# Performance work log

Hardware: AMD Instinct MI355X
Metric: run time of the kernel (lower is better)

## Reference

```python
import jax, jax.numpy as jnp
import numpy as np

B, D, C = 2048, 1024, 8192


def setup_inputs() -> dict:
    key = jax.random.key(0)
    k1, k2, k3 = jax.random.split(key, 3)
    x = jax.random.normal(k1, (B, D), dtype=jnp.float32)
    y = jax.random.randint(k2, (B,), 0, C)
    centroids = jax.random.normal(k3, (C, D), dtype=jnp.float32)
    return {"x": x, "y": y, "centroids": centroids}


def reference(x, y, centroids):
    x2 = jnp.sum(x * x, axis=-1, keepdims=True)          # (B, 1)
    c2 = jnp.sum(centroids * centroids, axis=-1)          # (C,)
    logits = -(x2 + c2[None, :] - 2.0 * (x @ centroids.T))  # (B, C)
    decisions = jnp.argmax(logits, axis=1)                # nearest centroid
    score = jnp.mean((decisions == y).astype(jnp.float32))
    # CrossEntropyLoss(distances, y)
    logp = jax.nn.log_softmax(logits, axis=-1)
    loss = -jnp.mean(jnp.take_along_axis(logp, y[:, None], axis=1))
    return loss, score
```

## Files before the change

kernel.cpp:

```cpp
#include <hip/hip_runtime.h>
#include <cstdint>

#define MDIM 2048
#define KDIM 1024
#define CDIM 8192
#define BM 128
#define BN 128
#define BK 32
#define NCHUNK (2 * (CDIM / BN))

typedef __attribute__((ext_vector_type(8))) __bf16 bf16x8;
typedef __attribute__((ext_vector_type(4))) float f32x4;

__device__ __forceinline__ unsigned short f2bf(float f) {
  unsigned u = __float_as_uint(f);
  u += 0x7fffu + ((u >> 16) & 1u);
  return (unsigned short)(u >> 16);
}

__device__ __forceinline__ void async_ld16(const void* g, void* l) {
  __builtin_amdgcn_global_load_lds(
      (__attribute__((address_space(1))) void*)(g),
      (__attribute__((address_space(3))) void*)(l),
      16, 0, 0);
}

__global__ __launch_bounds__(256) void convert_all(const float* __restrict__ x,
                                                   const float* __restrict__ cent,
                                                   unsigned short* __restrict__ xb,
                                                   unsigned short* __restrict__ cb,
                                                   float* __restrict__ c2) {
  const int b = blockIdx.x, t = threadIdx.x;
  if (b < MDIM) {
    const float4 v = ((const float4*)(x + (size_t)b * KDIM))[t];
    ushort4 o;
    o.x = f2bf(v.x); o.y = f2bf(v.y); o.z = f2bf(v.z); o.w = f2bf(v.w);
    ((ushort4*)(xb + (size_t)b * KDIM))[t] = o;
  } else {
    const int row = b - MDIM;
    const float4 v = ((const float4*)(cent + (size_t)row * KDIM))[t];
    ushort4 o;
    o.x = f2bf(v.x); o.y = f2bf(v.y); o.z = f2bf(v.z); o.w = f2bf(v.w);
    ((ushort4*)(cb + (size_t)row * KDIM))[t] = o;
    float p = v.x * v.x + v.y * v.y + v.z * v.z + v.w * v.w;
    for (int d = 32; d; d >>= 1) p += __shfl_down(p, d, 64);
    __shared__ float red[4];
    if ((t & 63) == 0) red[t >> 6] = p;
    __syncthreads();
    if (t == 0) c2[row] = red[0] + red[1] + red[2] + red[3];
  }
}

__global__ __launch_bounds__(256) void gemm_reduce(
    const unsigned short* __restrict__ Ab, const unsigned short* __restrict__ Bb,
    const float* __restrict__ c2,
    float* __restrict__ pm, float* __restrict__ pl, int* __restrict__ pidx) {
  __shared__ __align__(16) unsigned short As[BM * BK];
  __shared__ __align__(16) unsigned short Bs[BN * BK];
  const int tid = threadIdx.x;
  const int wave = tid >> 6, lane = tid & 63;
  const int wm = wave >> 1, wn = wave & 1;
  const int bn = blockIdx.x, bm = blockIdx.y;
  const int quad = lane >> 4, c16 = lane & 15;

  f32x4 acc[4][4] = {};

  const int srow = lane >> 2;
  const int scol = (lane & 3) * 8;
  const unsigned short* ag = Ab + (size_t)(bm * BM + wave * 32 + srow) * KDIM + scol;
  const unsigned short* bg = Bb + (size_t)(bn * BN + wave * 32 + srow) * KDIM + scol;
  unsigned short* asl = &As[(wave * 32) * BK];
  unsigned short* bsl = &Bs[(wave * 32) * BK];

  for (int k0 = 0; k0 < KDIM; k0 += BK) {
    async_ld16(ag + k0, asl);
    async_ld16(ag + k0 + 16 * KDIM, asl + 16 * BK);
    async_ld16(bg + k0, bsl);
    async_ld16(bg + k0 + 16 * KDIM, bsl + 16 * BK);
    __syncthreads();
    bf16x8 a[4], b[4];
#pragma unroll
    for (int mt = 0; mt < 4; ++mt)
      a[mt] = *(const bf16x8*)&As[(wm * 64 + mt * 16 + c16) * BK + quad * 8];
#pragma unroll
    for (int nt = 0; nt < 4; ++nt)
      b[nt] = *(const bf16x8*)&Bs[(wn * 64 + nt * 16 + c16) * BK + quad * 8];
#pragma unroll
    for (int mt = 0; mt < 4; ++mt)
#pragma unroll
      for (int nt = 0; nt < 4; ++nt)
        acc[mt][nt] = __builtin_amdgcn_mfma_f32_16x16x32_bf16(a[mt], b[nt], acc[mt][nt], 0, 0, 0);
    __syncthreads();
  }

  const int colbase = bn * BN + wn * 64;
  float c2v[4];
#pragma unroll
  for (int nt = 0; nt < 4; ++nt) c2v[nt] = c2[colbase + nt * 16 + c16];

  const int chunk = bn * 2 + wn;
#pragma unroll
  for (int mt = 0; mt < 4; ++mt) {
#pragma unroll
    for (int r = 0; r < 4; ++r) {
      float sv[4];
#pragma unroll
      for (int nt = 0; nt < 4; ++nt) sv[nt] = 2.0f * acc[mt][nt][r] - c2v[nt];
      float m = sv[0];
      int idx = colbase + c16;
#pragma unroll
      for (int nt = 1; nt < 4; ++nt) {
        if (sv[nt] > m) { m = sv[nt]; idx = colbase + nt * 16 + c16; }
      }
      float l = 0.f;
#pragma unroll
      for (int nt = 0; nt < 4; ++nt) l += __expf(sv[nt] - m);
      for (int d = 1; d < 16; d <<= 1) {
        float om = __shfl_xor(m, d, 64);
        float ol = __shfl_xor(l, d, 64);
        int oi = __shfl_xor(idx, d, 64);
        float M = fmaxf(m, om);
        l = l * __expf(m - M) + ol * __expf(om - M);
        idx = (om > m || (om == m && oi < idx)) ? oi : idx;
        m = M;
      }
      if (c16 == 0) {
        const int row = bm * BM + wm * 64 + mt * 16 + quad * 4 + r;
        pm[(size_t)row * NCHUNK + chunk] = m;
        pl[(size_t)row * NCHUNK + chunk] = l;
        pidx[(size_t)row * NCHUNK + chunk] = idx;
      }
    }
  }
}

__global__ __launch_bounds__(128) void combine_kernel(
    const float* __restrict__ pm, const float* __restrict__ pl,
    const int* __restrict__ pidx, const float* __restrict__ x,
    const float* __restrict__ cent, const float* __restrict__ c2,
    const int* __restrict__ y,
    float* __restrict__ loss_part, float* __restrict__ corr_part) {
  const int row = blockIdx.x, t = threadIdx.x;
  const int yc = y[row];

  float m = pm[(size_t)row * NCHUNK + t];
  float l = pl[(size_t)row * NCHUNK + t];
  int idx = pidx[(size_t)row * NCHUNK + t];

  const float4* xa = (const float4*)(x + (size_t)row * KDIM) + t * 2;
  const float4* ca = (const float4*)(cent + (size_t)yc * KDIM) + t * 2;
  const float4 a0 = xa[0], a1 = xa[1], b0 = ca[0], b1 = ca[1];
  float dot = a0.x * b0.x + a0.y * b0.y + a0.z * b0.z + a0.w * b0.w
            + a1.x * b1.x + a1.y * b1.y + a1.z * b1.z + a1.w * b1.w;

  for (int d = 1; d < 64; d <<= 1) {
    const float om = __shfl_xor(m, d, 64);
    const float ol = __shfl_xor(l, d, 64);
    const int oi = __shfl_xor(idx, d, 64);
    const float od = __shfl_xor(dot, d, 64);
    const float M = fmaxf(m, om);
    l = l * __expf(m - M) + ol * __expf(om - M);
    idx = (om > m || (om == m && oi < idx)) ? oi : idx;
    m = M;
    dot += od;
  }
  __shared__ float sm[2], sl[2], sd[2];
  __shared__ int si[2];
  if ((t & 63) == 0) { sm[t >> 6] = m; sl[t >> 6] = l; si[t >> 6] = idx; sd[t >> 6] = dot; }
  __syncthreads();
  if (t == 0) {
    const float m0 = sm[0], m1 = sm[1];
    const float M = fmaxf(m0, m1);
    const float L = sl[0] * __expf(m0 - M) + sl[1] * __expf(m1 - M);
    int g;
    if (m1 > m0 || (m1 == m0 && si[1] < si[0])) g = si[1]; else g = si[0];
    const float sy = 2.0f * (sd[0] + sd[1]) - c2[yc];
    loss_part[row] = __logf(L) + M - sy;
    corr_part[row] = (g == yc) ? 1.f : 0.f;
  }
}

__global__ __launch_bounds__(256) void finalize(const float* __restrict__ loss_part,
                                                const float* __restrict__ corr_part,
                                                float* __restrict__ out) {
  const int t = threadIdx.x;
  float s0 = 0.f, s1 = 0.f;
  for (int i = t; i < MDIM; i += 256) { s0 += loss_part[i]; s1 += corr_part[i]; }
  for (int d = 32; d; d >>= 1) {
    s0 += __shfl_down(s0, d, 64);
    s1 += __shfl_down(s1, d, 64);
  }
  __shared__ float r0[4], r1[4];
  if ((t & 63) == 0) { r0[t >> 6] = s0; r1[t >> 6] = s1; }
  __syncthreads();
  if (t == 0) {
    out[0] = (r0[0] + r0[1] + r0[2] + r0[3]) * (1.0f / MDIM);
    out[1] = (r1[0] + r1[1] + r1[2] + r1[3]) * (1.0f / MDIM);
  }
}

extern "C" void kernel_launch(void* const* d_in, const int* in_sizes, int n_in,
                              void* d_out, int out_size, void* d_ws, size_t ws_size,
                              hipStream_t stream) {
  const float* x = (const float*)d_in[0];
  const int* y = (const int*)d_in[1];
  const float* cent = (const float*)d_in[2];
  float* out = (float*)d_out;

  char* ws = (char*)d_ws;
  const size_t OFF_XB = 0;
  const size_t OFF_CB = OFF_XB + (size_t)MDIM * KDIM * 2;
  const size_t OFF_C2 = OFF_CB + (size_t)CDIM * KDIM * 2;
  const size_t OFF_PM = OFF_C2 + (size_t)CDIM * 4;
  const size_t OFF_PL = OFF_PM + (size_t)NCHUNK * MDIM * 4;
  const size_t OFF_PI = OFF_PL + (size_t)NCHUNK * MDIM * 4;
  const size_t OFF_LP = OFF_PI + (size_t)NCHUNK * MDIM * 4;
  const size_t OFF_CP = OFF_LP + (size_t)MDIM * 4;
  const size_t NEED = OFF_CP + (size_t)MDIM * 4;
  if (ws_size < NEED) return;

  unsigned short* xb = (unsigned short*)(ws + OFF_XB);
  unsigned short* cb = (unsigned short*)(ws + OFF_CB);
  float* c2 = (float*)(ws + OFF_C2);
  float* pm = (float*)(ws + OFF_PM);
  float* pl = (float*)(ws + OFF_PL);
  int* pidx = (int*)(ws + OFF_PI);
  float* loss_part = (float*)(ws + OFF_LP);
  float* corr_part = (float*)(ws + OFF_CP);

  convert_all<<<MDIM + CDIM, 256, 0, stream>>>(x, cent, xb, cb, c2);
  gemm_reduce<<<dim3(CDIM / BN, MDIM / BM), 256, 0, stream>>>(xb, cb, c2, pm, pl, pidx);
  combine_kernel<<<MDIM, 128, 0, stream>>>(pm, pl, pidx, x, cent, c2, y, loss_part, corr_part);
  finalize<<<1, 256, 0, stream>>>(loss_part, corr_part, out);
}
```

Baseline: 153.6 us.

## Use 256x256 tiles with 4-stage async LDS pipeline, swizzle, and block remap

The GEMM moves to 256x256 block tiles with 512 threads. A 4-deep ring of LDS buffers is filled by asynchronous global-to-LDS loads three steps ahead, with explicit vmcnt waits and a single barrier per k-step, so memory latency overlaps MFMA work. LDS rows use an XOR swizzle to avoid bank conflicts, and the block index is remapped so that neighbouring blocks share tiles in L2. NCHUNK stays at 128, so combine is unchanged. The costs are 128KB of LDS, larger register use and fewer blocks in the grid (256 blocks).

```diff
diff --git a/kernel.cpp b/kernel.cpp
--- a/kernel.cpp
+++ b/kernel.cpp
@@ -4,10 +4,11 @@
 #define MDIM 2048
 #define KDIM 1024
 #define CDIM 8192
-#define BM 128
-#define BN 128
+#define BM 256
+#define BN 256
 #define BK 32
-#define NCHUNK (2 * (CDIM / BN))
+#define NT (KDIM / BK)
+#define NCHUNK (CDIM / 64)
 
 typedef __attribute__((ext_vector_type(8))) __bf16 bf16x8;
 typedef __attribute__((ext_vector_type(4))) float f32x4;
@@ -51,56 +52,93 @@
   }
 }
 
-__global__ __launch_bounds__(256) void gemm_reduce(
+__global__ __launch_bounds__(512, 2) void gemm_reduce(
     const unsigned short* __restrict__ Ab, const unsigned short* __restrict__ Bb,
     const float* __restrict__ c2,
     float* __restrict__ pm, float* __restrict__ pl, int* __restrict__ pidx) {
-  __shared__ __align__(16) unsigned short As[BM * BK];
-  __shared__ __align__(16) unsigned short Bs[BN * BK];
+  __shared__ __align__(16) char lds[4 * 32768];
+
   const int tid = threadIdx.x;
   const int wave = tid >> 6, lane = tid & 63;
-  const int wm = wave >> 1, wn = wave & 1;
-  const int bn = blockIdx.x, bm = blockIdx.y;
+  const int wm = wave >> 2, wn = wave & 3;
   const int quad = lane >> 4, c16 = lane & 15;
 
-  f32x4 acc[4][4] = {};
-
-  const int srow = lane >> 2;
-  const int scol = (lane & 3) * 8;
-  const unsigned short* ag = Ab + (size_t)(bm * BM + wave * 32 + srow) * KDIM + scol;
-  const unsigned short* bg = Bb + (size_t)(bn * BN + wave * 32 + srow) * KDIM + scol;
-  unsigned short* asl = &As[(wave * 32) * BK];
-  unsigned short* bsl = &Bs[(wave * 32) * BK];
-
-  for (int k0 = 0; k0 < KDIM; k0 += BK) {
-    async_ld16(ag + k0, asl);
-    async_ld16(ag + k0 + 16 * KDIM, asl + 16 * BK);
-    async_ld16(bg + k0, bsl);
-    async_ld16(bg + k0 + 16 * KDIM, bsl + 16 * BK);
-    __syncthreads();
-    bf16x8 a[4], b[4];
-#pragma unroll
-    for (int mt = 0; mt < 4; ++mt)
-      a[mt] = *(const bf16x8*)&As[(wm * 64 + mt * 16 + c16) * BK + quad * 8];
-#pragma unroll
-    for (int nt = 0; nt < 4; ++nt)
-      b[nt] = *(const bf16x8*)&Bs[(wn * 64 + nt * 16 + c16) * BK + quad * 8];
-#pragma unroll
-    for (int mt = 0; mt < 4; ++mt)
+  const int id = blockIdx.y * gridDim.x + blockIdx.x;
+  const int lid = (id & 7) * 32 + (id >> 3);
+  const int bm = lid >> 5, bn = lid & 31;
+  const int bmBase = bm * BM, bnBase = bn * BN;
+
+  const int r1 = tid >> 2, c1 = (tid & 3) ^ ((r1 >> 1) & 3);
+  const int r2 = (tid + 512) >> 2, c2s = (tid & 3) ^ ((r2 >> 1) & 3);
+  const char* Ag1 = (const char*)(Ab + (size_t)(bmBase + r1) * KDIM + c1 * 8);
+  const char* Ag2 = (const char*)(Ab + (size_t)(bmBase + r2) * KDIM + c2s * 8);
+  const char* Bg1 = (const char*)(Bb + (size_t)(bnBase + r1) * KDIM + c1 * 8);
+  const char* Bg2 = (const char*)(Bb + (size_t)(bnBase + r2) * KDIM + c2s * 8);
+  const int wbyte = wave * 1024;
+
+  int aoff[8], boff[4];
+#pragma unroll
+  for (int mt = 0; mt < 8; ++mt) {
+    const int row = wm * 128 + mt * 16 + c16;
+    aoff[mt] = row * 64 + ((quad ^ ((row >> 1) & 3)) * 16);
+  }
+#pragma unroll
+  for (int nt = 0; nt < 4; ++nt) {
+    const int col = wn * 64 + nt * 16 + c16;
+    boff[nt] = col * 64 + ((quad ^ ((col >> 1) & 3)) * 16);
+  }
+
+  f32x4 acc[8][4] = {};
+
+#define STAGE(T)                                          \
+  {                                                       \
+    const int _ko = (T) * (BK * 2);                       \
+    char* _sb = &lds[((T) & 3) * 32768];                  \
+    async_ld16(Ag1 + _ko, _sb + wbyte);                   \
+    async_ld16(Ag2 + _ko, _sb + 8192 + wbyte);            \
+    async_ld16(Bg1 + _ko, _sb + 16384 + wbyte);           \
+    async_ld16(Bg2 + _ko, _sb + 24576 + wbyte);           \
+  }
+
+  STAGE(0); STAGE(1); STAGE(2);
+
+#pragma unroll 1
+  for (int t = 0; t < NT; ++t) {
+    if (t < NT - 2)       asm volatile("s_waitcnt vmcnt(8)" ::: "memory");
+    else if (t == NT - 2) asm volatile("s_waitcnt vmcnt(4)" ::: "memory");
+    else                  asm volatile("s_waitcnt vmcnt(0)" ::: "memory");
+    __builtin_amdgcn_s_barrier();
+    __builtin_amdgcn_sched_barrier(0);
+
+    const char* sb = &lds[(t & 3) * 32768];
+    bf16x8 a[8], b[4];
+#pragma unroll
+    for (int mt = 0; mt < 8; ++mt) a[mt] = *(const bf16x8*)(sb + aoff[mt]);
+#pragma unroll
+    for (int nt = 0; nt < 4; ++nt) b[nt] = *(const bf16x8*)(sb + 16384 + boff[nt]);
+
+    if (t < NT - 3) STAGE(t + 3);
+
+    asm volatile("s_waitcnt lgkmcnt(0)" ::: "memory");
+    __builtin_amdgcn_sched_barrier(0);
+    __builtin_amdgcn_s_setprio(1);
+#pragma unroll
+    for (int mt = 0; mt < 8; ++mt)
 #pragma unroll
       for (int nt = 0; nt < 4; ++nt)
         acc[mt][nt] = __builtin_amdgcn_mfma_f32_16x16x32_bf16(a[mt], b[nt], acc[mt][nt], 0, 0, 0);
-    __syncthreads();
-  }
-
-  const int colbase = bn * BN + wn * 64;
+    __builtin_amdgcn_s_setprio(0);
+  }
+#undef STAGE
+
+  const int colbase = bnBase + wn * 64;
   float c2v[4];
 #pragma unroll
   for (int nt = 0; nt < 4; ++nt) c2v[nt] = c2[colbase + nt * 16 + c16];
 
-  const int chunk = bn * 2 + wn;
-#pragma unroll
-  for (int mt = 0; mt < 4; ++mt) {
+  const int chunk = bn * 4 + wn;
+#pragma unroll
+  for (int mt = 0; mt < 8; ++mt) {
 #pragma unroll
     for (int r = 0; r < 4; ++r) {
       float sv[4];
@@ -125,7 +163,7 @@
         m = M;
       }
       if (c16 == 0) {
-        const int row = bm * BM + wm * 64 + mt * 16 + quad * 4 + r;
+        const int row = bmBase + wm * 128 + mt * 16 + quad * 4 + r;
         pm[(size_t)row * NCHUNK + chunk] = m;
         pl[(size_t)row * NCHUNK + chunk] = l;
         pidx[(size_t)row * NCHUNK + chunk] = idx;
@@ -229,7 +267,7 @@
   float* corr_part = (float*)(ws + OFF_CP);
 
   convert_all<<<MDIM + CDIM, 256, 0, stream>>>(x, cent, xb, cb, c2);
-  gemm_reduce<<<dim3(CDIM / BN, MDIM / BM), 256, 0, stream>>>(xb, cb, c2, pm, pl, pidx);
+  gemm_reduce<<<dim3(CDIM / BN, MDIM / BM), 512, 0, stream>>>(xb, cb, c2, pm, pl, pidx);
   combine_kernel<<<MDIM, 128, 0, stream>>>(pm, pl, pidx, x, cent, c2, y, loss_part, corr_part);
   finalize<<<1, 256, 0, stream>>>(loss_part, corr_part, out);
 }
```

New measurement: 138.3 us. -9.9%, faster.
